# Performance work log

Hardware: AMD Instinct MI355X
Metric: run time of the kernel (lower is better)

Reference implementation:

```python
import jax, jax.numpy as jnp
import numpy as np

B, T, F, H = 64, 512, 132, 1024


def setup_inputs() -> dict:
    key = jax.random.key(0)
    ks = jax.random.split(key, 16)
    k = 1.0 / np.sqrt(H)
    u = lambda kk, shape: jax.random.uniform(kk, shape, jnp.float32, -k, k)
    return {
        "real_seq": jax.random.normal(ks[0], (B, T, F), jnp.float32),
        "Wih1": u(ks[1], (4 * H, F)), "Whh1": u(ks[2], (4 * H, H)),
        "bih1": u(ks[3], (4 * H,)), "bhh1": u(ks[4], (4 * H,)),
        "Wih2": u(ks[5], (4 * H, H)), "Whh2": u(ks[6], (4 * H, H)),
        "bih2": u(ks[7], (4 * H,)), "bhh2": u(ks[8], (4 * H,)),
        "Wih3": u(ks[9], (4 * H, H)), "Whh3": u(ks[10], (4 * H, H)),
        "bih3": u(ks[11], (4 * H,)), "bhh3": u(ks[12], (4 * H,)),
        "Wd": u(ks[13], (F, H)), "bd": u(ks[14], (F,)),
        "condition_num": 5, "groundtruth_num": 5,
    }


def _cell(x, h, c, Wih, Whh, bih, bhh):
    # torch LSTMCell gate order: i, f, g, o
    gates = x @ Wih.T + h @ Whh.T + bih + bhh
    i, f, g, o = jnp.split(gates, 4, axis=-1)
    c_new = jax.nn.sigmoid(f) * c + jax.nn.sigmoid(i) * jnp.tanh(g)
    h_new = jax.nn.sigmoid(o) * jnp.tanh(c_new)
    return h_new, c_new


def reference(real_seq, Wih1, Whh1, bih1, bhh1, Wih2, Whh2, bih2, bhh2,
              Wih3, Whh3, bih3, bhh3, Wd, bd, condition_num, groundtruth_num):
    batch, seq_len, _ = real_seq.shape
    hid = Whh1.shape[1]
    out_dim = Wd.shape[0]
    # static teacher-forcing schedule (numpy, as in get_condition_lst)
    gt = np.ones((100, groundtruth_num))
    con = np.zeros((100, condition_num))
    cond = jnp.asarray(np.concatenate((gt, con), 1).reshape(-1)[:seq_len],
                       jnp.float32)

    def step(carry, xs):
        h0, h1, h2, c0, c1, c2, prev_out = carry
        frame, flag = xs
        in_frame = jnp.where(flag == 1.0, frame, prev_out)
        # NOTE: faithful to source -- lstm2 gets OLD h0, lstm3 gets OLD h1
        h0n, c0n = _cell(in_frame, h0, c0, Wih1, Whh1, bih1, bhh1)
        h1n, c1n = _cell(h0, h1, c1, Wih2, Whh2, bih2, bhh2)
        h2n, c2n = _cell(h1, h2, c2, Wih3, Whh3, bih3, bhh3)
        out = h2n @ Wd.T + bd
        return (h0n, h1n, h2n, c0n, c1n, c2n, out), out

    z = jnp.zeros((batch, hid), real_seq.dtype)
    out0 = jnp.zeros((batch, out_dim), real_seq.dtype)
    _, outs = jax.lax.scan(step, (z, z, z, z, z, z, out0),
                           (jnp.swapaxes(real_seq, 0, 1), cond))
    # outs: [T, B, F] -> concat along feature axis per timestep: [B, T*F]
    return jnp.transpose(outs, (1, 0, 2)).reshape(batch, seq_len * out_dim)
```

## Files before the change

### kernel.cpp

```cpp
#include <hip/hip_runtime.h>
#include <cstdint>


#define NBLK 256
#define NTHR 512
#define Bn 64
#define Tn 512
#define Fn 132
#define Hn 1024
#define TF (Tn * Fn)
#define SRCH 65536
#define HBUF 196608
#define XTT 10240
#define WPB 102400
#define STB 393216
#define STU 49152

typedef _Float16 h8 __attribute__((ext_vector_type(8)));
typedef float f4 __attribute__((ext_vector_type(4)));
typedef int v4i __attribute__((ext_vector_type(4)));
typedef unsigned long long ull;

__device__ v4i llvm_amdgcn_raw_buffer_load_v4i32(v4i srsrc, int voffset,
                                                 int soffset, int aux)
    __asm("llvm.amdgcn.raw.buffer.load.v4i32");

__device__ __forceinline__ v4i make_srd(const void* p) {
    union { struct { unsigned lo, hi, sz, cfg; } s; v4i v; } u;
    u.s.lo = (unsigned)(uintptr_t)p;
    u.s.hi = (unsigned)((uintptr_t)p >> 32);
    u.s.sz = 0xFFFFFFFFu;
    u.s.cfg = 0x00020000u;
    return u.v;
}

__device__ __forceinline__ h8 bload16(v4i rsrc, int voff) {
    union { v4i i; h8 h; } c;
    c.i = llvm_amdgcn_raw_buffer_load_v4i32(rsrc, voff, 0, 1 );
    return c.h;
}

__device__ __forceinline__ float sigf(float x) { return 1.0f / (1.0f + expf(-x)); }

__device__ __forceinline__ ull cload8(const void* p) {
    return __hip_atomic_load((const ull*)p, __ATOMIC_RELAXED, __HIP_MEMORY_SCOPE_AGENT);
}
__device__ __forceinline__ void cstore8(void* p, ull v) {
    __hip_atomic_store((ull*)p, v, __ATOMIC_RELAXED, __HIP_MEMORY_SCOPE_AGENT);
}

__device__ __forceinline__ void garrive(unsigned* bar, unsigned ep) {
    unsigned* cnt = bar + ((blockIdx.x >> 5) << 5);
    unsigned old = __hip_atomic_fetch_add(cnt, 1u, __ATOMIC_RELAXED,
                                          __HIP_MEMORY_SCOPE_AGENT);
    if (old == 32u * ep - 1u) {
        unsigned d = __hip_atomic_fetch_add(bar + 256, 1u, __ATOMIC_RELAXED,
                                            __HIP_MEMORY_SCOPE_AGENT);
        if (d == 8u * ep - 1u)
            __hip_atomic_store(bar + 288, ep, __ATOMIC_RELAXED,
                               __HIP_MEMORY_SCOPE_AGENT);
    }
}
__device__ __forceinline__ void gwait(unsigned* bar, unsigned ep) {
    while (__hip_atomic_load(bar + 288, __ATOMIC_RELAXED,
                             __HIP_MEMORY_SCOPE_AGENT) < ep)
        __builtin_amdgcn_s_sleep(1);
}
__device__ __forceinline__ void gsyncA(unsigned* bar, unsigned ep) {
    __syncthreads();
    if (threadIdx.x == 0) { garrive(bar, ep); gwait(bar, ep); }
    __syncthreads();
}


__global__ void k_bsum(const float* bih1, const float* bhh1, const float* bih2,
                       const float* bhh2, const float* bih3, const float* bhh3,
                       const float* Wih1, const float* bd,
                       float* bsum, float* bsum2) {
    int i = blockIdx.x * 256 + threadIdx.x;
    if (i < NBLK * 48) {
        int bidw = i / 48, r = i % 48;
        int cell = r >> 4, n = r & 15;
        int row = (n >> 2) * Hn + bidw * 4 + (n & 3);
        const float* bi = cell == 0 ? bih1 : (cell == 1 ? bih2 : bih3);
        const float* bh = cell == 0 ? bhh1 : (cell == 1 ? bhh2 : bhh3);
        bsum[i] = bi[row] + bh[row];
    } else if (i < NBLK * 64) {
        int ii = i - NBLK * 48;
        int bidw = ii / 16, n = ii % 16;
        int row = (n >> 2) * Hn + bidw * 4 + (n & 3);
        float s = 0.0f;
        for (int f = 0; f < Fn; ++f) s += Wih1[(size_t)row * Fn + f] * bd[f];
        bsum2[bidw * 16 + n] = s;
    }
}

__global__ void k_convx(const float* xseq, _Float16* xT) {
    int i = blockIdx.x * 256 + threadIdx.x;
    if (i >= Tn * XTT) return;
    int t = i / XTT, r = i % XTT;
    int k8 = r >> 9, b = (r >> 3) & 63, e = r & 7;
    int f = k8 * 8 + e;
    float v = (f < Fn) ? xseq[((size_t)b * Tn + t) * Fn + f] : 0.0f;
    xT[i] = (_Float16)v;
}

__global__ void k_convw(const float* Wih1, const float* Whh1, const float* Wih2,
                        const float* Whh2, const float* Wih3, const float* Whh3,
                        const float* Wd, _Float16* wblob) {
    int i = blockIdx.x * 256 + threadIdx.x;
    if (i >= NBLK * WPB) return;
    int bidw = i / WPB, r = i % WPB;
    int slot = r >> 9, e = r & 511;
    int w = slot / 25, s = slot - w * 25;
    int l = e >> 3, j = e & 7;
    int kq = l >> 4, n = l & 15;
    int row = (n >> 2) * Hn + bidw * 4 + (n & 3);
    float v = 0.0f;
    if (s >= 21) {
        int kt = w * 4 + (s - 21);
        int k = kt * 32 + kq * 8 + j;
        float acc = 0.0f;
        for (int f = 0; f < Fn; ++f)
            acc += Wih1[(size_t)row * Fn + f] * Wd[(size_t)f * Hn + k];
        v = acc;
    } else {
        const float* M;
        int K, kt;
        if (s < 4)       { M = Whh1; K = Hn; kt = w * 4 + s; }
        else if (s < 8)  { M = Wih2; K = Hn; kt = w * 4 + s - 4; }
        else if (s < 12) { M = Whh2; K = Hn; kt = w * 4 + s - 8; }
        else if (s < 16) { M = Wih3; K = Hn; kt = w * 4 + s - 12; }
        else if (s < 20) { M = Whh3; K = Hn; kt = w * 4 + s - 16; }
        else             { M = Wih1; K = Fn; kt = w; }
        int k = kt * 32 + kq * 8 + j;
        if (!(s == 20 && w >= 5) && k < K) v = M[(size_t)row * K + k];
    }
    wblob[i] = (_Float16)v;
}

__global__ void k_misc(_Float16* hT) {
    int i = blockIdx.x * 256 + threadIdx.x;
    if (i < HBUF) hT[i] = (_Float16)0.0f;
}


__global__ __launch_bounds__(NTHR, 2) void lstm_mfma(
    const _Float16* __restrict__ xT, const _Float16* __restrict__ wblob,
    _Float16* __restrict__ hT, unsigned char* __restrict__ xstage,
    const float* __restrict__ bsum, const float* __restrict__ bsum2,
    const float* __restrict__ Wd, const float* __restrict__ bd,
    const int* __restrict__ cnum_p, const int* __restrict__ gnum_p,
    float* __restrict__ dout, unsigned* __restrict__ bar) {
    __shared__ float red[8 * 12 * 68 * 4];
    __shared__ float cst[768];
    __shared__ float sbias[48];
    __shared__ float sbias2[16];
    __shared__ unsigned long long hstage[192];
    __shared__ int sxi[3];

    const int tid = threadIdx.x;
    const int bid = blockIdx.x;
    const int lane = tid & 63;
    const int wid = tid >> 6;
    const int laneAB = (lane >> 4) * 1024 + (lane & 15) * 16;
    const int laneA0 = (lane >> 4) * 512 + (lane & 15) * 8;
    const int widB = wid * 16384;

    if (tid < 48) sbias[tid] = bsum[bid * 48 + tid];
    if (tid >= 64 && tid < 80) sbias2[tid - 64] = bsum2[bid * 16 + (tid - 64)];
    for (int i = tid; i < 768; i += NTHR) cst[i] = 0.0f;

    h8 wfr[25];
    {
        const _Float16* wp = wblob + (size_t)bid * WPB + (size_t)(wid * 25) * 512 + lane * 8;
#pragma unroll
        for (int s2 = 0; s2 < 25; ++s2) wfr[s2] = *(const h8*)(wp + s2 * 512);
    }

    if (tid == 0) {
        unsigned x;
        asm volatile("s_getreg_b32 %0, hwreg(HW_REG_XCC_ID)" : "=s"(x));
        x &= 7u;
        unsigned r = __hip_atomic_fetch_add(bar + 384 + x * 16, 1u,
                                            __ATOMIC_RELAXED, __HIP_MEMORY_SCOPE_AGENT);
        sxi[0] = (int)x; sxi[1] = (int)r;
    }
    gsyncA(bar, 1);
    if (tid == 0)
        sxi[2] = (int)__hip_atomic_load(bar + 384 + sxi[0] * 16, __ATOMIC_RELAXED,
                                        __HIP_MEMORY_SCOPE_AGENT);
    __syncthreads();
    const int xcd = sxi[0], xrank = sxi[1], xN = sxi[2];
    unsigned* xb = bar + 640 + xcd * 16;
    unsigned char* xsb = xstage + (size_t)xcd * 2 * STB;

    const int gnum = gnum_p[0];
    const int per = gnum + cnum_p[0];

    auto decoder = [&](v4i rsrc, int tt) {
        const int ss = tid >> 6, b = tid & 63;
        const int nj = (bid < 8) ? 2 : 1;
        for (int j2 = 0; j2 < nj; ++j2) {
            int f, half;
            if (j2 == 0) {
                if (bid < Fn) { f = bid; half = 0; }
                else          { f = bid - Fn; half = 1; }
            } else { f = bid + (NBLK - Fn); half = 1; }
            const float* wdr = Wd + (size_t)f * Hn;
            float p = 0.0f;
#pragma unroll
            for (int i = 0; i < 8; ++i) {
                const int k8 = half * 64 + ss * 8 + i;
                h8 hv = bload16(rsrc, 262144 + k8 * 1024 + b * 16);
                const float4 w0 = *(const float4*)(wdr + k8 * 8);
                const float4 w1 = *(const float4*)(wdr + k8 * 8 + 4);
                p = fmaf((float)hv[0], w0.x, p); p = fmaf((float)hv[1], w0.y, p);
                p = fmaf((float)hv[2], w0.z, p); p = fmaf((float)hv[3], w0.w, p);
                p = fmaf((float)hv[4], w1.x, p); p = fmaf((float)hv[5], w1.y, p);
                p = fmaf((float)hv[6], w1.z, p); p = fmaf((float)hv[7], w1.w, p);
            }
            red[ss * 64 + b] = p;
            __syncthreads();
            if (tid < 64) {
                float o = (half == 0) ? bd[f] : 0.0f;
#pragma unroll
                for (int u = 0; u < 8; ++u) o += red[u * 64 + tid];
                unsafeAtomicAdd(&dout[(size_t)tid * TF + (size_t)tt * Fn + f], o);
            }
            __syncthreads();
        }
    };

    auto stage = [&](int rbuf, int slot) {
        const ull* src = (const ull*)(hT + (size_t)rbuf * HBUF);
        ull* dst = (ull*)(xsb + (size_t)slot * STB);
        for (int s2 = xrank; s2 < 32; s2 += xN) {
            const int u = s2 * 1536 + tid;
#pragma unroll
            for (int q = 0; q < 3; ++q)
                dst[u + q * 512] = cload8(src + u + q * 512);
        }
        __syncthreads();
    };
    auto xsync = [&](unsigned target) {
        if (tid == 0) {
            __hip_atomic_fetch_add(xb, 1u, __ATOMIC_RELAXED, __HIP_MEMORY_SCOPE_AGENT);
            while (__hip_atomic_load(xb, __ATOMIC_RELAXED, __HIP_MEMORY_SCOPE_AGENT) < target)
                __builtin_amdgcn_s_sleep(1);
        }
        __syncthreads();
    };

    int tmod = 0;
    for (int t = 0; t < Tn; ++t) {
        const int flag = (tmod < gnum) ? 1 : 0;
        const bool fused = (!flag) && (t > 0);
        const int rb = t % 3, wb2 = (t + 1) % 3;
        _Float16* hw = hT + (size_t)wb2 * HBUF;

        stage(rb, t & 1);
        xsync((unsigned)(xN * (t + 1)));
        const v4i rsrc = make_srd(xsb + (size_t)(t & 1) * STB);

        f4 acc[12];
#pragma unroll
        for (int i = 0; i < 12; ++i) acc[i] = (f4){0.f, 0.f, 0.f, 0.f};

        if (flag && wid < 5) {
            const _Float16* x0 = xT + (size_t)t * XTT + wid * 2048 + laneA0;
#pragma unroll
            for (int mt = 0; mt < 4; ++mt) {
                h8 a = *(const h8*)(x0 + mt * 128);
                acc[mt] = __builtin_amdgcn_mfma_f32_16x16x32_f16(a, wfr[20], acc[mt], 0, 0, 0);
            }
        }
#pragma unroll
        for (int i2 = 0; i2 < 4; ++i2) {
#pragma unroll
            for (int mt = 0; mt < 4; ++mt) {
                h8 a = bload16(rsrc, widB + i2 * 4096 + mt * 256 + laneAB);
                acc[mt]     = __builtin_amdgcn_mfma_f32_16x16x32_f16(a, wfr[i2],     acc[mt],     0, 0, 0);
                acc[4 + mt] = __builtin_amdgcn_mfma_f32_16x16x32_f16(a, wfr[4 + i2], acc[4 + mt], 0, 0, 0);
            }
        }
#pragma unroll
        for (int i2 = 0; i2 < 4; ++i2) {
#pragma unroll
            for (int mt = 0; mt < 4; ++mt) {
                h8 a = bload16(rsrc, 131072 + widB + i2 * 4096 + mt * 256 + laneAB);
                acc[4 + mt] = __builtin_amdgcn_mfma_f32_16x16x32_f16(a, wfr[8 + i2],  acc[4 + mt], 0, 0, 0);
                acc[8 + mt] = __builtin_amdgcn_mfma_f32_16x16x32_f16(a, wfr[12 + i2], acc[8 + mt], 0, 0, 0);
            }
        }
        if (fused) {
#pragma unroll
            for (int i2 = 0; i2 < 4; ++i2) {
#pragma unroll
                for (int mt = 0; mt < 4; ++mt) {
                    h8 a = bload16(rsrc, 262144 + widB + i2 * 4096 + mt * 256 + laneAB);
                    acc[8 + mt] = __builtin_amdgcn_mfma_f32_16x16x32_f16(a, wfr[16 + i2], acc[8 + mt], 0, 0, 0);
                    acc[mt]     = __builtin_amdgcn_mfma_f32_16x16x32_f16(a, wfr[21 + i2], acc[mt],     0, 0, 0);
                }
            }
        } else {
#pragma unroll
            for (int i2 = 0; i2 < 4; ++i2) {
#pragma unroll
                for (int mt = 0; mt < 4; ++mt) {
                    h8 a = bload16(rsrc, 262144 + widB + i2 * 4096 + mt * 256 + laneAB);
                    acc[8 + mt] = __builtin_amdgcn_mfma_f32_16x16x32_f16(a, wfr[16 + i2], acc[8 + mt], 0, 0, 0);
                }
            }
        }

        {
            float* wr = red + ((size_t)(wid * 12) * 68 + (lane >> 4) * 17 + (lane & 15)) * 4;
#pragma unroll
            for (int cc = 0; cc < 3; ++cc)
#pragma unroll
                for (int mt = 0; mt < 4; ++mt)
                    *(f4*)(wr + (cc * 4 + mt) * 68 * 4) = acc[cc * 4 + mt];
        }
        __syncthreads();
        const float bmul = fused ? 1.0f : 0.0f;
        for (int idx = tid; idx < 768; idx += NTHR) {
            const int cell = idx >> 8, jj = (idx >> 6) & 3, b = idx & 63;
            const int mt = b >> 4, mq = (b >> 2) & 3, rr = b & 3;
            float gv4[4];
#pragma unroll
            for (int gt = 0; gt < 4; ++gt) {
                const int n = gt * 4 + jj;
                float v = sbias[cell * 16 + n];
                if (cell == 0) v += bmul * sbias2[n];
#pragma unroll
                for (int w2 = 0; w2 < 8; ++w2)
                    v += red[(((w2 * 12 + cell * 4 + mt)) * 68 + mq * 17 + n) * 4 + rr];
                gv4[gt] = v;
            }
            const float cold = cst[(cell * 4 + jj) * 64 + b];
            const float cn = sigf(gv4[1]) * cold + sigf(gv4[0]) * tanhf(gv4[2]);
            cst[(cell * 4 + jj) * 64 + b] = cn;
            const float hn = sigf(gv4[3]) * tanhf(cn);
            ((_Float16*)hstage)[(cell * 64 + b) * 4 + jj] = (_Float16)hn;
        }
        __syncthreads();
        if (tid < 192) {
            const int cell = tid >> 6, b = tid & 63;
            _Float16* dst = hw + cell * SRCH + (bid >> 1) * 512 + b * 8 + 4 * (bid & 1);
            cstore8(dst, hstage[tid]);
        }

        __syncthreads();
        if (tid == 0) garrive(bar, (unsigned)(t + 2));
        if (t > 0) decoder(rsrc, t - 1);
        __syncthreads();
        if (tid == 0) gwait(bar, (unsigned)(t + 2));
        __syncthreads();

        tmod = (tmod + 1 >= per) ? 0 : (tmod + 1);
    }

    stage(Tn % 3, Tn & 1);
    xsync((unsigned)(xN * (Tn + 1)));
    decoder(make_srd(xsb + (size_t)(Tn & 1) * STB), Tn - 1);
}


extern "C" void kernel_launch(void* const* d_in, const int* in_sizes, int n_in,
                              void* d_out, int out_size, void* d_ws, size_t ws_size,
                              hipStream_t stream) {
    const float* xseq = (const float*)d_in[0];
    const float* Wih1 = (const float*)d_in[1];
    const float* Whh1 = (const float*)d_in[2];
    const float* bih1 = (const float*)d_in[3];
    const float* bhh1 = (const float*)d_in[4];
    const float* Wih2 = (const float*)d_in[5];
    const float* Whh2 = (const float*)d_in[6];
    const float* bih2 = (const float*)d_in[7];
    const float* bhh2 = (const float*)d_in[8];
    const float* Wih3 = (const float*)d_in[9];
    const float* Whh3 = (const float*)d_in[10];
    const float* bih3 = (const float*)d_in[11];
    const float* bhh3 = (const float*)d_in[12];
    const float* Wd = (const float*)d_in[13];
    const float* bd = (const float*)d_in[14];
    const int* cnum_p = (const int*)d_in[15];
    const int* gnum_p = (const int*)d_in[16];

    unsigned char* ws = (unsigned char*)d_ws;
    unsigned* bar = (unsigned*)ws;
    float* bsum = (float*)(ws + 4096);
    float* bsum2 = (float*)(ws + 53248);
    _Float16* xT = (_Float16*)(ws + 102400);
    _Float16* wblob = (_Float16*)(ws + 102400 + 10485760);
    _Float16* hT = (_Float16*)(ws + 102400 + 10485760 + 52428800);
    unsigned char* xstage = ws + 102400 + 10485760 + 52428800 + 1179648;

    hipMemsetAsync(bar, 0, 4096, stream);
    hipMemsetAsync(d_out, 0, (size_t)out_size * sizeof(float), stream);
    hipLaunchKernelGGL(k_bsum, dim3((NBLK * 64 + 255) / 256), dim3(256), 0, stream,
                       bih1, bhh1, bih2, bhh2, bih3, bhh3, Wih1, bd, bsum, bsum2);
    hipLaunchKernelGGL(k_convx, dim3((Tn * XTT + 255) / 256), dim3(256), 0, stream,
                       xseq, xT);
    hipLaunchKernelGGL(k_convw, dim3((NBLK * WPB + 255) / 256), dim3(256), 0, stream,
                       Wih1, Whh1, Wih2, Whh2, Wih3, Whh3, Wd, wblob);
    hipLaunchKernelGGL(k_misc, dim3((HBUF + 255) / 256), dim3(256), 0, stream, hT);
    hipLaunchKernelGGL(lstm_mfma, dim3(NBLK), dim3(NTHR), 0, stream,
                       xT, wblob, hT, xstage, bsum, bsum2, Wd, bd, cnum_p, gnum_p,
                       (float*)d_out, bar);
}
```

Before: 7.712 ms.

## Split XCD barrier into arrive/poll and batch loads ahead of MFMAs

The per-XCD staging barrier is split into an arrive and a poll, so the input-frame MFMA work runs between them and hides barrier latency. The first staging loads are issued before the accumulators are zeroed, overlapping global-load latency. Operand loads for each gate block, and the decoder's hidden-state loads, are grouped ahead of their MFMA/FMA chains for more memory-level parallelism. This raises register pressure, which could lower occupancy or cause spills.

```diff
diff --git a/kernel.cpp b/kernel.cpp
--- a/kernel.cpp
+++ b/kernel.cpp
@@ -208,17 +208,22 @@
                 else          { f = bid - Fn; half = 1; }
             } else { f = bid + (NBLK - Fn); half = 1; }
             const float* wdr = Wd + (size_t)f * Hn;
-            float p = 0.0f;
+            h8 hv[8];
 #pragma unroll
             for (int i = 0; i < 8; ++i) {
                 const int k8 = half * 64 + ss * 8 + i;
-                h8 hv = bload16(rsrc, 262144 + k8 * 1024 + b * 16);
+                hv[i] = bload16(rsrc, 262144 + k8 * 1024 + b * 16);
+            }
+            float p = 0.0f;
+#pragma unroll
+            for (int i = 0; i < 8; ++i) {
+                const int k8 = half * 64 + ss * 8 + i;
                 const float4 w0 = *(const float4*)(wdr + k8 * 8);
                 const float4 w1 = *(const float4*)(wdr + k8 * 8 + 4);
-                p = fmaf((float)hv[0], w0.x, p); p = fmaf((float)hv[1], w0.y, p);
-                p = fmaf((float)hv[2], w0.z, p); p = fmaf((float)hv[3], w0.w, p);
-                p = fmaf((float)hv[4], w1.x, p); p = fmaf((float)hv[5], w1.y, p);
-                p = fmaf((float)hv[6], w1.z, p); p = fmaf((float)hv[7], w1.w, p);
+                p = fmaf((float)hv[i][0], w0.x, p); p = fmaf((float)hv[i][1], w0.y, p);
+                p = fmaf((float)hv[i][2], w0.z, p); p = fmaf((float)hv[i][3], w0.w, p);
+                p = fmaf((float)hv[i][4], w1.x, p); p = fmaf((float)hv[i][5], w1.y, p);
+                p = fmaf((float)hv[i][6], w1.z, p); p = fmaf((float)hv[i][7], w1.w, p);
             }
             red[ss * 64 + b] = p;
             __syncthreads();
@@ -232,7 +237,7 @@
         }
     };
 
-    auto stage = [&](int rbuf, int slot) {
+    auto stageT = [&](int rbuf, int slot) {
         const ull* src = (const ull*)(hT + (size_t)rbuf * HBUF);
         ull* dst = (ull*)(xsb + (size_t)slot * STB);
         for (int s2 = xrank; s2 < 32; s2 += xN) {
@@ -243,12 +248,14 @@
         }
         __syncthreads();
     };
-    auto xsync = [&](unsigned target) {
-        if (tid == 0) {
+    auto xarrive = [&]() {
+        if (tid == 0)
             __hip_atomic_fetch_add(xb, 1u, __ATOMIC_RELAXED, __HIP_MEMORY_SCOPE_AGENT);
+    };
+    auto xpoll = [&](unsigned target) {
+        if (tid == 0)
             while (__hip_atomic_load(xb, __ATOMIC_RELAXED, __HIP_MEMORY_SCOPE_AGENT) < target)
                 __builtin_amdgcn_s_sleep(1);
-        }
         __syncthreads();
     };
 
@@ -259,58 +266,92 @@
         const int rb = t % 3, wb2 = (t + 1) % 3;
         _Float16* hw = hT + (size_t)wb2 * HBUF;
 
-        stage(rb, t & 1);
-        xsync((unsigned)(xN * (t + 1)));
-        const v4i rsrc = make_srd(xsb + (size_t)(t & 1) * STB);
-
+        const ull* ssrc = (const ull*)(hT + (size_t)rb * HBUF);
+        ull* sdst = (ull*)(xsb + (size_t)(t & 1) * STB);
+        ull sv0 = 0, sv1 = 0, sv2 = 0;
+        int u0 = -1;
+        if (xrank < 32) {
+            u0 = xrank * 1536 + tid;
+            sv0 = cload8(ssrc + u0);
+            sv1 = cload8(ssrc + u0 + 512);
+            sv2 = cload8(ssrc + u0 + 1024);
+        }
         f4 acc[12];
 #pragma unroll
         for (int i = 0; i < 12; ++i) acc[i] = (f4){0.f, 0.f, 0.f, 0.f};
+        if (u0 >= 0) { sdst[u0] = sv0; sdst[u0 + 512] = sv1; sdst[u0 + 1024] = sv2; }
+        for (int s2 = xrank + xN; s2 < 32; s2 += xN) {
+            const int u = s2 * 1536 + tid;
+#pragma unroll
+            for (int q = 0; q < 3; ++q)
+                sdst[u + q * 512] = cload8(ssrc + u + q * 512);
+        }
+        __syncthreads();
+        xarrive();
 
         if (flag && wid < 5) {
             const _Float16* x0 = xT + (size_t)t * XTT + wid * 2048 + laneA0;
-#pragma unroll
-            for (int mt = 0; mt < 4; ++mt) {
-                h8 a = *(const h8*)(x0 + mt * 128);
-                acc[mt] = __builtin_amdgcn_mfma_f32_16x16x32_f16(a, wfr[20], acc[mt], 0, 0, 0);
-            }
-        }
-#pragma unroll
-        for (int i2 = 0; i2 < 4; ++i2) {
-#pragma unroll
-            for (int mt = 0; mt < 4; ++mt) {
-                h8 a = bload16(rsrc, widB + i2 * 4096 + mt * 256 + laneAB);
-                acc[mt]     = __builtin_amdgcn_mfma_f32_16x16x32_f16(a, wfr[i2],     acc[mt],     0, 0, 0);
-                acc[4 + mt] = __builtin_amdgcn_mfma_f32_16x16x32_f16(a, wfr[4 + i2], acc[4 + mt], 0, 0, 0);
-            }
-        }
-#pragma unroll
-        for (int i2 = 0; i2 < 4; ++i2) {
-#pragma unroll
-            for (int mt = 0; mt < 4; ++mt) {
-                h8 a = bload16(rsrc, 131072 + widB + i2 * 4096 + mt * 256 + laneAB);
-                acc[4 + mt] = __builtin_amdgcn_mfma_f32_16x16x32_f16(a, wfr[8 + i2],  acc[4 + mt], 0, 0, 0);
-                acc[8 + mt] = __builtin_amdgcn_mfma_f32_16x16x32_f16(a, wfr[12 + i2], acc[8 + mt], 0, 0, 0);
-            }
-        }
-        if (fused) {
-#pragma unroll
-            for (int i2 = 0; i2 < 4; ++i2) {
+            h8 xa[4];
+#pragma unroll
+            for (int mt = 0; mt < 4; ++mt) xa[mt] = *(const h8*)(x0 + mt * 128);
+#pragma unroll
+            for (int mt = 0; mt < 4; ++mt)
+                acc[mt] = __builtin_amdgcn_mfma_f32_16x16x32_f16(xa[mt], wfr[20], acc[mt], 0, 0, 0);
+        }
+        xpoll((unsigned)(xN * (t + 1)));
+        const v4i rsrc = make_srd(xsb + (size_t)(t & 1) * STB);
+
+        {
+            h8 a[16];
+#pragma unroll
+            for (int i2 = 0; i2 < 4; ++i2)
+#pragma unroll
+                for (int mt = 0; mt < 4; ++mt)
+                    a[i2 * 4 + mt] = bload16(rsrc, widB + i2 * 4096 + mt * 256 + laneAB);
+#pragma unroll
+            for (int i2 = 0; i2 < 4; ++i2)
 #pragma unroll
                 for (int mt = 0; mt < 4; ++mt) {
-                    h8 a = bload16(rsrc, 262144 + widB + i2 * 4096 + mt * 256 + laneAB);
-                    acc[8 + mt] = __builtin_amdgcn_mfma_f32_16x16x32_f16(a, wfr[16 + i2], acc[8 + mt], 0, 0, 0);
-                    acc[mt]     = __builtin_amdgcn_mfma_f32_16x16x32_f16(a, wfr[21 + i2], acc[mt],     0, 0, 0);
+                    acc[mt]     = __builtin_amdgcn_mfma_f32_16x16x32_f16(a[i2 * 4 + mt], wfr[i2],     acc[mt],     0, 0, 0);
+                    acc[4 + mt] = __builtin_amdgcn_mfma_f32_16x16x32_f16(a[i2 * 4 + mt], wfr[4 + i2], acc[4 + mt], 0, 0, 0);
                 }
-            }
-        } else {
-#pragma unroll
-            for (int i2 = 0; i2 < 4; ++i2) {
+        }
+        {
+            h8 a[16];
+#pragma unroll
+            for (int i2 = 0; i2 < 4; ++i2)
+#pragma unroll
+                for (int mt = 0; mt < 4; ++mt)
+                    a[i2 * 4 + mt] = bload16(rsrc, 131072 + widB + i2 * 4096 + mt * 256 + laneAB);
+#pragma unroll
+            for (int i2 = 0; i2 < 4; ++i2)
 #pragma unroll
                 for (int mt = 0; mt < 4; ++mt) {
-                    h8 a = bload16(rsrc, 262144 + widB + i2 * 4096 + mt * 256 + laneAB);
-                    acc[8 + mt] = __builtin_amdgcn_mfma_f32_16x16x32_f16(a, wfr[16 + i2], acc[8 + mt], 0, 0, 0);
+                    acc[4 + mt] = __builtin_amdgcn_mfma_f32_16x16x32_f16(a[i2 * 4 + mt], wfr[8 + i2],  acc[4 + mt], 0, 0, 0);
+                    acc[8 + mt] = __builtin_amdgcn_mfma_f32_16x16x32_f16(a[i2 * 4 + mt], wfr[12 + i2], acc[8 + mt], 0, 0, 0);
                 }
+        }
+        {
+            h8 a[16];
+#pragma unroll
+            for (int i2 = 0; i2 < 4; ++i2)
+#pragma unroll
+                for (int mt = 0; mt < 4; ++mt)
+                    a[i2 * 4 + mt] = bload16(rsrc, 262144 + widB + i2 * 4096 + mt * 256 + laneAB);
+            if (fused) {
+#pragma unroll
+                for (int i2 = 0; i2 < 4; ++i2)
+#pragma unroll
+                    for (int mt = 0; mt < 4; ++mt) {
+                        acc[8 + mt] = __builtin_amdgcn_mfma_f32_16x16x32_f16(a[i2 * 4 + mt], wfr[16 + i2], acc[8 + mt], 0, 0, 0);
+                        acc[mt]     = __builtin_amdgcn_mfma_f32_16x16x32_f16(a[i2 * 4 + mt], wfr[21 + i2], acc[mt],     0, 0, 0);
+                    }
+            } else {
+#pragma unroll
+                for (int i2 = 0; i2 < 4; ++i2)
+#pragma unroll
+                    for (int mt = 0; mt < 4; ++mt)
+                        acc[8 + mt] = __builtin_amdgcn_mfma_f32_16x16x32_f16(a[i2 * 4 + mt], wfr[16 + i2], acc[8 + mt], 0, 0, 0);
             }
         }
 
@@ -361,8 +402,14 @@
         tmod = (tmod + 1 >= per) ? 0 : (tmod + 1);
     }
 
-    stage(Tn % 3, Tn & 1);
-    xsync((unsigned)(xN * (Tn + 1)));
+    stageT(Tn % 3, Tn & 1);
+    if (tid == 0) {
+        __hip_atomic_fetch_add(xb, 1u, __ATOMIC_RELAXED, __HIP_MEMORY_SCOPE_AGENT);
+        while (__hip_atomic_load(xb, __ATOMIC_RELAXED, __HIP_MEMORY_SCOPE_AGENT)
+               < (unsigned)(xN * (Tn + 1)))
+            __builtin_amdgcn_s_sleep(1);
+    }
+    __syncthreads();
     decoder(make_srd(xsb + (size_t)(Tn & 1) * STB), Tn - 1);
 }
 
```

Measured after the change: 7.791 ms. About the same (+1.0%).
